# Optimization experiments

Hardware: AMD Instinct MI355X
Metric: run time of the kernel (lower is better)

## Reference

```python
import jax, jax.numpy as jnp
import numpy as np

SPH, SPW = 24, 24          # spatial tile size
NBLK = 2                   # channel blocks (in_channels // 512)
EPS = 1e-5


def _tiles(h, w):
    nh = int(np.ceil(h / SPH)); nw = int(np.ceil(w / SPW))
    sh = (h - SPH) // (nh - 1) if nh > 1 else 0
    sw = (w - SPW) // (nw - 1) if nw > 1 else 0
    offs = []
    for i in range(nh):
        for j in range(nw):
            offs.append((max(0, i * sh), max(0, j * sw)))
    return offs, nh, nw


def _mlp(x_v, w1, b1, w2, b2):
    # 1x1 conv1d pair over the spatial_area axis: x_v (B, S, C)
    h = jax.nn.relu(jnp.einsum('os,bsc->boc', w1, x_v) + b1[None, :, None])
    return jnp.einsum('so,boc->bsc', w2, h) + b2[None, :, None]


def _forward(x, w_in1, b_in1, w_in2, b_in2, w_out1, b_out1, w_out2, b_out2, bn_gamma, bn_beta):
    bt, c, h, w = x.shape
    offs, nh, nw = _tiles(h, w)
    # gather overlapping (here exactly tiling) spatial patches -> stacked chunk batch
    chunks = [x[:, :, ty:ty + SPH, tx:tx + SPW].reshape(bt, c, SPH * SPW) for ty, tx in offs]
    x_stacked = jnp.concatenate(chunks, 0)            # (nchunks*bt, c, S)
    x_v = jnp.transpose(x_stacked, (0, 2, 1))         # (B, S, c)
    x_v = _mlp(x_v, w_in1, b_in1, w_in2, b_in2)
    # negative squared-distance score over channel means (no detach in this branch)
    x_m = x_v.mean(axis=1)                            # (B, c)
    score = -(x_m[:, None, :] - x_m[:, :, None]) ** 2  # (B, c, c)
    blk = c // NBLK
    ids = jnp.arange(c) // blk
    mask = ids[:, None] == ids[None, :]               # block-diagonal channel mask
    score = jnp.where(mask[None], score, -jnp.inf)
    attn = jax.nn.softmax(score, axis=1)              # softmax over dim 1 (rows)
    out = jnp.einsum('bsc,bcd->bsd', x_v, attn)       # torch.bmm(x_v, attn)
    out = _mlp(out, w_out1, b_out1, w_out2, b_out2)
    # BatchNorm1d(spatial_area) in training mode: stats over (B, c) per S-channel
    mu = out.mean(axis=(0, 2), keepdims=True)
    var = out.var(axis=(0, 2), keepdims=True)
    out = (out - mu) * jax.lax.rsqrt(var + EPS) * bn_gamma[None, :, None] + bn_beta[None, :, None]
    out = jnp.transpose(out, (0, 2, 1))               # (B, c, S)
    # scatter_add chunks back (scaled by 1/spblock_h^2, as in the original)
    scale = 1.0 / (nh * nh)
    res = x
    for idx, (ty, tx) in enumerate(offs):
        chunk = out[idx * bt:(idx + 1) * bt].reshape(bt, c, SPH, SPW)
        res = res.at[:, :, ty:ty + SPH, tx:tx + SPW].add(chunk * scale)
    return jax.nn.relu(res)


def setup_inputs() -> dict:
    key = jax.random.key(0)
    ks = jax.random.split(key, 9)
    S = SPH * SPW          # 576
    H = S // 8             # 72 (reduction=8)
    s = 0.02
    return {
        'x': jax.random.normal(ks[0], (16, 1024, 48, 48), dtype=jnp.float32),
        'w_in1': jax.random.normal(ks[1], (H, S), dtype=jnp.float32) * s,
        'b_in1': jnp.zeros((H,), jnp.float32),
        'w_in2': jax.random.normal(ks[2], (S, H), dtype=jnp.float32) * s,
        'b_in2': jnp.zeros((S,), jnp.float32),
        'w_out1': jax.random.normal(ks[3], (H, S), dtype=jnp.float32) * s,
        'b_out1': jnp.zeros((H,), jnp.float32),
        'w_out2': jax.random.normal(ks[4], (S, H), dtype=jnp.float32) * s,
        'b_out2': jnp.zeros((S,), jnp.float32),
        'bn_gamma': jnp.ones((S,), jnp.float32),
        'bn_beta': jnp.zeros((S,), jnp.float32),
    }


def reference(x, w_in1, b_in1, w_in2, b_in2, w_out1, b_out1, w_out2, b_out2, bn_gamma, bn_beta):
    return _forward(x, w_in1, b_in1, w_in2, b_in2, w_out1, b_out1, w_out2, b_out2, bn_gamma, bn_beta)
```

## Files before the change

kernel.cpp:

```cpp
#include <hip/hip_runtime.h>
#include <hip/hip_bf16.h>


#define EPS 1e-5f

typedef __attribute__((ext_vector_type(8))) short short8;
typedef __attribute__((ext_vector_type(4))) short short4v;
typedef __attribute__((ext_vector_type(4))) float f32x4;
typedef __attribute__((ext_vector_type(4))) float float4v;

#define GLD_LDS(g, l) __builtin_amdgcn_global_load_lds( \
    (const __attribute__((address_space(1))) void*)(g), \
    (__attribute__((address_space(3))) void*)(l), 16, 0, 0)

static __device__ __forceinline__ unsigned short f2bu(float f) {
    union { __hip_bfloat16 h; unsigned short u; } cv;
    cv.h = __float2bfloat16(f);
    return cv.u;
}

__global__ void prep_k(const float* __restrict__ w_in1, const float* __restrict__ b_in1,
                       const float* __restrict__ w_in2,
                       const float* __restrict__ w_out1, const float* __restrict__ b_out1,
                       const float* __restrict__ w_out2,
                       __hip_bfloat16* __restrict__ w1p, __hip_bfloat16* __restrict__ w1op,
                       __hip_bfloat16* __restrict__ w2p, __hip_bfloat16* __restrict__ w2op,
                       float* __restrict__ b1p, float* __restrict__ b1op)
{
    int i = blockIdx.x * 256 + threadIdx.x;
    if (i < 128 * 576) {
        int r = i / 576, c = i - r * 576;
        w1p[i]  = __float2bfloat16(r < 72 ? w_in1[r * 576 + c] : 0.f);
        w1op[i] = __float2bfloat16(r < 72 ? w_out1[r * 576 + c] : 0.f);
    }
    if (i < 640 * 96) {
        int r = i / 96, c = i - r * 96;
        bool ok = (r < 576) && (c < 72);
        w2p[i]  = __float2bfloat16(ok ? w_in2[r * 72 + c] : 0.f);
        w2op[i] = __float2bfloat16(ok ? w_out2[r * 72 + c] : 0.f);
    }
    if (i < 128) {
        b1p[i]  = i < 72 ? b_in1[i] : 0.f;
        b1op[i] = i < 72 ? b_out1[i] : 0.f;
    }
}

__global__ void extract_k(const float4v* __restrict__ x4, __hip_bfloat16* __restrict__ xv)
{
    int i = blockIdx.x * 256 + threadIdx.x;
    int s4 = i % 144;
    int m = i / 144;
    int c = m & 1023;
    int b = m >> 10;
    int n = b & 15, ti = b >> 4;
    int ty = (ti >> 1) * 24, tx = (ti & 1) * 24;
    int s = s4 * 4;
    int sy = s / 24, sx = s - sy * 24;
    float4v v = x4[((((n << 10) + c) * 48 + ty + sy) * 48 + tx + sx) >> 2];
    short4v pk;
    pk.x = (short)f2bu(v.x); pk.y = (short)f2bu(v.y);
    pk.z = (short)f2bu(v.z); pk.w = (short)f2bu(v.w);
    *(short4v*)(xv + (long)i * 4) = pk;
}

template<int MODE>
__global__ __launch_bounds__(256) void fused_mlp(
    const unsigned short* __restrict__ A,
    const unsigned short* __restrict__ W1,
    const float* __restrict__ b1,
    const unsigned short* __restrict__ W2,
    const float* __restrict__ b2,
    __hip_bfloat16* __restrict__ xv1T,
    float* __restrict__ xm_raw,
    __hip_bfloat16* __restrict__ C,
    float* __restrict__ statsR)
{
    constexpr int SMEM_SH = (MODE == 0) ? 38016 : 21504;
    __shared__ __align__(16) unsigned short smem[SMEM_SH];
    unsigned short* As = smem;
    unsigned short* Bs = smem + 4096;
    unsigned short* Hs = smem + 8192;
    unsigned short* T  = smem + 21504;

    const int m0 = blockIdx.x * 128;
    const int t = threadIdx.x;
    const int lane = t & 63, wave = t >> 6;
    const int wr = wave >> 1, wc = wave & 1;
    const int lrow = lane & 15, kq = (lane >> 4) * 8;
    const int cr = (lane >> 4) * 4;
    const int r0 = t >> 2, c0 = (t & 3) * 8;

    f32x4 acc[4][4];
    #pragma unroll
    for (int i = 0; i < 4; ++i)
        #pragma unroll
        for (int j = 0; j < 4; ++j)
            acc[i][j] = (f32x4){0.f, 0.f, 0.f, 0.f};

    for (int k0 = 0; k0 < 576; k0 += 32) {
        GLD_LDS(A + (long)(m0 + r0) * 576 + k0 + c0,      &As[t * 8]);
        GLD_LDS(A + (long)(m0 + r0 + 64) * 576 + k0 + c0, &As[(t + 256) * 8]);
        GLD_LDS(W1 + (long)r0 * 576 + k0 + c0,            &Bs[t * 8]);
        GLD_LDS(W1 + (long)(r0 + 64) * 576 + k0 + c0,     &Bs[(t + 256) * 8]);
        __syncthreads();
        short8 af[4], bf[4];
        #pragma unroll
        for (int i = 0; i < 4; ++i)
            af[i] = *(const short8*)&As[(wr * 64 + i * 16 + lrow) * 32 + kq];
        #pragma unroll
        for (int j = 0; j < 4; ++j)
            bf[j] = *(const short8*)&Bs[(wc * 64 + j * 16 + lrow) * 32 + kq];
        #pragma unroll
        for (int i = 0; i < 4; ++i)
            #pragma unroll
            for (int j = 0; j < 4; ++j)
                acc[i][j] = __builtin_amdgcn_mfma_f32_16x16x32_bf16(af[i], bf[j], acc[i][j], 0, 0, 0);
        __syncthreads();
    }

    #pragma unroll
    for (int j = 0; j < 4; ++j) {
        int col = wc * 64 + j * 16 + lrow;
        if (col < 96) {
            float bv = b1[col];
            #pragma unroll
            for (int i = 0; i < 4; ++i) {
                int row = wr * 64 + i * 16 + cr;
                #pragma unroll
                for (int r = 0; r < 4; ++r)
                    Hs[(row + r) * 104 + col] = f2bu(fmaxf(acc[i][j][r] + bv, 0.f));
            }
        }
    }
    __syncthreads();

    float rsum[4][4];
    if (MODE == 0)
        #pragma unroll
        for (int i = 0; i < 4; ++i)
            #pragma unroll
            for (int r = 0; r < 4; ++r)
                rsum[i][r] = 0.f;

    const int z = m0 >> 9, m_local = m0 & 511;

    for (int n0 = 0; n0 < 640; n0 += 128) {
        f32x4 a2[4][4];
        #pragma unroll
        for (int i = 0; i < 4; ++i)
            #pragma unroll
            for (int j = 0; j < 4; ++j)
                a2[i][j] = (f32x4){0.f, 0.f, 0.f, 0.f};

        for (int k0 = 0; k0 < 96; k0 += 32) {
            GLD_LDS(W2 + (long)(n0 + r0) * 96 + k0 + c0,      &Bs[t * 8]);
            GLD_LDS(W2 + (long)(n0 + r0 + 64) * 96 + k0 + c0, &Bs[(t + 256) * 8]);
            __syncthreads();
            short8 af[4], bf[4];
            #pragma unroll
            for (int i = 0; i < 4; ++i)
                af[i] = *(const short8*)&Hs[(wr * 64 + i * 16 + lrow) * 104 + k0 + kq];
            #pragma unroll
            for (int j = 0; j < 4; ++j)
                bf[j] = *(const short8*)&Bs[(wc * 64 + j * 16 + lrow) * 32 + kq];
            #pragma unroll
            for (int i = 0; i < 4; ++i)
                #pragma unroll
                for (int j = 0; j < 4; ++j)
                    a2[i][j] = __builtin_amdgcn_mfma_f32_16x16x32_bf16(af[i], bf[j], a2[i][j], 0, 0, 0);
            __syncthreads();
        }

        if (MODE == 0) {
            #pragma unroll
            for (int i = 0; i < 4; ++i)
                #pragma unroll
                for (int r = 0; r < 4; ++r)
                    rsum[i][r] += a2[i][0][r] + a2[i][1][r] + a2[i][2][r] + a2[i][3][r];

            #pragma unroll
            for (int j = 0; j < 4; ++j) {
                int col = wc * 64 + j * 16 + lrow;
                float bv = (n0 + col < 576) ? b2[n0 + col] : 0.f;
                #pragma unroll
                for (int i = 0; i < 4; ++i) {
                    int row = wr * 64 + i * 16 + cr;
                    #pragma unroll
                    for (int r = 0; r < 4; ++r)
                        T[(row + r) * 129 + col] = f2bu(a2[i][j][r] + bv);
                }
            }
            __syncthreads();

            int s_r = t >> 1, chalf = (t & 1) * 64;
            if (n0 + s_r < 576) {
                __hip_bfloat16* dst = xv1T + ((long)z * 640 + n0 + s_r) * 512 + m_local + chalf;
                #pragma unroll
                for (int v8 = 0; v8 < 8; ++v8) {
                    short8 pk;
                    #pragma unroll
                    for (int e = 0; e < 8; ++e)
                        pk[e] = (short)T[(chalf + v8 * 8 + e) * 129 + s_r];
                    *(short8*)(dst + v8 * 8) = pk;
                }
            }
            __syncthreads();
        } else {
            float* st = statsR + (blockIdx.x & 7) * 1152;
            #pragma unroll
            for (int j = 0; j < 4; ++j) {
                int col = n0 + wc * 64 + j * 16 + lrow;
                bool live = col < 576;
                float bv = live ? b2[col] : 0.f;
                float s1 = 0.f, s2 = 0.f;
                #pragma unroll
                for (int i = 0; i < 4; ++i) {
                    long rowb = (long)(m0 + wr * 64 + i * 16 + cr) * 576;
                    #pragma unroll
                    for (int r = 0; r < 4; ++r) {
                        float v = a2[i][j][r] + bv;
                        s1 += v; s2 += v * v;
                        if (live) C[rowb + (long)r * 576 + col] = __float2bfloat16(v);
                    }
                }
                s1 += __shfl_xor(s1, 16, 64); s1 += __shfl_xor(s1, 32, 64);
                s2 += __shfl_xor(s2, 16, 64); s2 += __shfl_xor(s2, 32, 64);
                if ((lane >> 4) == 0 && live) {
                    atomicAdd(&st[col], s1);
                    atomicAdd(&st[576 + col], s2);
                }
            }
        }
    }

    if (MODE == 0) {
        #pragma unroll
        for (int i = 0; i < 4; ++i)
            #pragma unroll
            for (int r = 0; r < 4; ++r) {
                float v = rsum[i][r];
                v += __shfl_xor(v, 1, 64);
                v += __shfl_xor(v, 2, 64);
                v += __shfl_xor(v, 4, 64);
                v += __shfl_xor(v, 8, 64);
                if (lrow == 0)
                    atomicAdd(&xm_raw[m0 + wr * 64 + i * 16 + cr + r], v);
            }
    }
}

__global__ void denom_k(const float* __restrict__ xm_raw, const float* __restrict__ b_in2,
                        float* __restrict__ xmn, float* __restrict__ invd)
{
    __shared__ float sx[512];
    __shared__ float red[256];
    int z = blockIdx.x;
    int t = threadIdx.x;
    float p = 0.f;
    for (int i = t; i < 576; i += 256) p += b_in2[i];
    red[t] = p; __syncthreads();
    for (int o = 128; o; o >>= 1) { if (t < o) red[t] += red[t + o]; __syncthreads(); }
    float btot = red[0];
    for (int i = t; i < 512; i += 256) {
        float m = (xm_raw[(long)z * 512 + i] + btot) * (1.f / 576.f);
        sx[i] = m;
        xmn[(long)z * 512 + i] = m;
    }
    __syncthreads();
    #pragma unroll
    for (int dd = 0; dd < 2; ++dd) {
        int d = t + dd * 256;
        float xd = sx[d], s = 0.f;
        for (int c = 0; c < 512; ++c) { float df = sx[c] - xd; s += __expf(-df * df); }
        invd[(long)z * 512 + d] = 1.f / s;
    }
}

__global__ __launch_bounds__(256) void gemm_attn(
    const unsigned short* __restrict__ Bg,
    const float* __restrict__ xmn, const float* __restrict__ invd,
    __hip_bfloat16* __restrict__ C)
{
    __shared__ unsigned short As[128 * 32];
    __shared__ unsigned short Bs[128 * 32];
    __shared__ float sxm[512];
    __shared__ float sinv[128];
    int g = blockIdx.x;
    int xcd = g & 7, idx = g >> 3;
    int y = idx & 3;
    int combo = (idx >> 2) * 8 + xcd;
    int nx = combo % 5, z = combo / 5;
    const int m0 = y * 128, n0 = nx * 128;
    const int t = threadIdx.x;
    const int lane = t & 63, wave = t >> 6;
    const int wr = wave >> 1, wc = wave & 1;
    const int lrow = lane & 15, kq = (lane >> 4) * 8;
    const int r0 = t >> 2, c0 = (t & 3) * 8;
    const unsigned short* B = Bg + (long)z * 640 * 512;
    __hip_bfloat16* Cz = C + (long)z * 512 * 576;

    for (int i = t; i < 512; i += 256) sxm[i] = xmn[(long)z * 512 + i];
    if (t < 128) sinv[t] = invd[(long)z * 512 + m0 + t];
    __syncthreads();

    const int dA = t >> 1, cbA = (t & 1) * 16;
    const float xd = sxm[m0 + dA];
    const float ivd = sinv[dA];

    f32x4 acc[4][4];
    #pragma unroll
    for (int i = 0; i < 4; ++i)
        #pragma unroll
        for (int j = 0; j < 4; ++j)
            acc[i][j] = (f32x4){0.f, 0.f, 0.f, 0.f};

    for (int k0 = 0; k0 < 512; k0 += 32) {
        GLD_LDS(B + (long)(n0 + r0) * 512 + k0 + c0,      &Bs[t * 8]);
        GLD_LDS(B + (long)(n0 + r0 + 64) * 512 + k0 + c0, &Bs[(t + 256) * 8]);
        short8 pk0, pk1;
        #pragma unroll
        for (int e = 0; e < 8; ++e) {
            float d0 = sxm[k0 + cbA + e] - xd;
            pk0[e] = (short)f2bu(__expf(-d0 * d0) * ivd);
            float d1 = sxm[k0 + cbA + 8 + e] - xd;
            pk1[e] = (short)f2bu(__expf(-d1 * d1) * ivd);
        }
        *(short8*)&As[dA * 32 + cbA]     = pk0;
        *(short8*)&As[dA * 32 + cbA + 8] = pk1;
        __syncthreads();
        short8 af[4], bf[4];
        #pragma unroll
        for (int i = 0; i < 4; ++i)
            af[i] = *(const short8*)&As[(wr * 64 + i * 16 + lrow) * 32 + kq];
        #pragma unroll
        for (int j = 0; j < 4; ++j)
            bf[j] = *(const short8*)&Bs[(wc * 64 + j * 16 + lrow) * 32 + kq];
        #pragma unroll
        for (int i = 0; i < 4; ++i)
            #pragma unroll
            for (int j = 0; j < 4; ++j)
                acc[i][j] = __builtin_amdgcn_mfma_f32_16x16x32_bf16(af[i], bf[j], acc[i][j], 0, 0, 0);
        __syncthreads();
    }

    const int cr = (lane >> 4) * 4;
    #pragma unroll
    for (int j = 0; j < 4; ++j) {
        int col = n0 + wc * 64 + j * 16 + lrow;
        if (col >= 576) continue;
        #pragma unroll
        for (int i = 0; i < 4; ++i) {
            long rowb = (long)(m0 + wr * 64 + i * 16 + cr) * 576;
            #pragma unroll
            for (int r = 0; r < 4; ++r)
                Cz[rowb + (long)r * 576 + col] = __float2bfloat16(acc[i][j][r]);
        }
    }
}

__global__ void bnfin_k(const float* __restrict__ statsR,
                        const float* __restrict__ gamma, const float* __restrict__ beta,
                        float* __restrict__ ab)
{
    int s = threadIdx.x;
    float sum = 0.f, sq = 0.f;
    #pragma unroll
    for (int r = 0; r < 8; ++r) {
        sum += statsR[r * 1152 + s];
        sq  += statsR[r * 1152 + 576 + s];
    }
    float mu = sum * (1.f / 65536.f);
    float var = sq * (1.f / 65536.f) - mu * mu;
    float a = gamma[s] * rsqrtf(var + EPS);
    ab[s] = a;
    ab[576 + s] = beta[s] - mu * a;
}

__global__ void final_k(const float4v* __restrict__ x4, const __hip_bfloat16* __restrict__ out3,
                        const float* __restrict__ ab, float4v* __restrict__ out4)
{
    int i = blockIdx.x * 256 + threadIdx.x;
    int xx4 = i % 12; int t = i / 12;
    int y = t % 48; t /= 48;
    int c = t & 1023; int n = t >> 10;
    int xx = xx4 * 4;
    int ti = (y / 24) * 2 + (xx / 24);
    int b = ti * 16 + n;
    int s = (y % 24) * 24 + (xx % 24);
    const __hip_bfloat16* o3 = out3 + (((long)b << 10) + c) * 576 + s;
    float4v xv = x4[i];
    float4v o;
    #pragma unroll
    for (int e = 0; e < 4; ++e) {
        float v = __bfloat162float(o3[e]);
        float bn = v * ab[s + e] + ab[576 + s + e];
        float r = (e == 0 ? xv.x : e == 1 ? xv.y : e == 2 ? xv.z : xv.w) + 0.25f * bn;
        if (e == 0) o.x = fmaxf(r, 0.f);
        else if (e == 1) o.y = fmaxf(r, 0.f);
        else if (e == 2) o.z = fmaxf(r, 0.f);
        else o.w = fmaxf(r, 0.f);
    }
    out4[i] = o;
}

extern "C" void kernel_launch(void* const* d_in, const int* in_sizes, int n_in,
                              void* d_out, int out_size, void* d_ws, size_t ws_size,
                              hipStream_t stream)
{
    const float* x      = (const float*)d_in[0];
    const float* w_in1  = (const float*)d_in[1];
    const float* b_in1  = (const float*)d_in[2];
    const float* w_in2  = (const float*)d_in[3];
    const float* b_in2  = (const float*)d_in[4];
    const float* w_out1 = (const float*)d_in[5];
    const float* b_out1 = (const float*)d_in[6];
    const float* w_out2 = (const float*)d_in[7];
    const float* b_out2 = (const float*)d_in[8];
    const float* gamma  = (const float*)d_in[9];
    const float* beta   = (const float*)d_in[10];

    char* ws = (char*)d_ws;
    __hip_bfloat16* xv0    = (__hip_bfloat16*)(ws);
    __hip_bfloat16* out3   = (__hip_bfloat16*)(ws + 88080384L);
    __hip_bfloat16* xv1T   = (__hip_bfloat16*)(ws + 163577856L);
    float*          xmn    = (float*)(ws + 247463936L);
    float*          xm_raw = (float*)(ws + 247726080L);
    float*          invd   = (float*)(ws + 247988224L);
    float*          statsR = (float*)(ws + 248250368L);
    float*          ab     = (float*)(ws + 248287232L);
    __hip_bfloat16* w1p    = (__hip_bfloat16*)(ws + 248291840L);
    __hip_bfloat16* w1op   = (__hip_bfloat16*)(ws + 248439296L);
    __hip_bfloat16* w2p    = (__hip_bfloat16*)(ws + 248586752L);
    __hip_bfloat16* w2op   = (__hip_bfloat16*)(ws + 248709632L);
    float*          b1p    = (float*)(ws + 248832512L);
    float*          b1op   = (float*)(ws + 248833024L);
    __hip_bfloat16* out2   = xv0;

    hipMemsetAsync(xm_raw, 0, 262144, stream);
    hipMemsetAsync(statsR, 0, 36864, stream);

    prep_k<<<288, 256, 0, stream>>>(w_in1, b_in1, w_in2, w_out1, b_out1, w_out2,
                                    w1p, w1op, w2p, w2op, b1p, b1op);

    extract_k<<<36864, 256, 0, stream>>>((const float4v*)x, xv0);

    fused_mlp<0><<<512, 256, 0, stream>>>(
        (const unsigned short*)xv0, (const unsigned short*)w1p, b1p,
        (const unsigned short*)w2p, b_in2,
        xv1T, xm_raw, nullptr, nullptr);

    denom_k<<<128, 256, 0, stream>>>(xm_raw, b_in2, xmn, invd);

    gemm_attn<<<2560, 256, 0, stream>>>(
        (const unsigned short*)xv1T, xmn, invd, out2);

    fused_mlp<1><<<512, 256, 0, stream>>>(
        (const unsigned short*)out2, (const unsigned short*)w1op, b1op,
        (const unsigned short*)w2op, b_out2,
        nullptr, nullptr, out3, statsR);

    bnfin_k<<<1, 576, 0, stream>>>(statsR, gamma, beta, ab);

    final_k<<<36864, 256, 0, stream>>>((const float4v*)x, out3, ab, (float4v*)d_out);
}
```

Baseline: 562.9 us.

## Reassociate attention with output MLP first layer to shrink intermediate GEMM

The attention bmm is reassociated so that the first output-MLP weight (72x576) is applied to x_v before attention, producing a small 128x512 G matrix per chunk. The full 576x512 transposed x_v intermediate is no longer materialised, and the attention GEMM inner dimension drops from 576 to 128 rows. The attention GEMM is also fused with the second output-MLP layer and the BN statistics, which removes one kernel and one large bf16 round trip. The cost is an extra GEMM inside the first MLP kernel and more LDS per block, which may reduce occupancy.

```diff
diff --git a/kernel.cpp b/kernel.cpp
--- a/kernel.cpp
+++ b/kernel.cpp
@@ -23,21 +23,24 @@
                        const float* __restrict__ w_in2,
                        const float* __restrict__ w_out1, const float* __restrict__ b_out1,
                        const float* __restrict__ w_out2,
-                       __hip_bfloat16* __restrict__ w1p, __hip_bfloat16* __restrict__ w1op,
-                       __hip_bfloat16* __restrict__ w2p, __hip_bfloat16* __restrict__ w2op,
+                       __hip_bfloat16* __restrict__ w1p, __hip_bfloat16* __restrict__ w2p,
+                       __hip_bfloat16* __restrict__ w2op, __hip_bfloat16* __restrict__ w1oq,
                        float* __restrict__ b1p, float* __restrict__ b1op)
 {
     int i = blockIdx.x * 256 + threadIdx.x;
     if (i < 128 * 576) {
         int r = i / 576, c = i - r * 576;
-        w1p[i]  = __float2bfloat16(r < 72 ? w_in1[r * 576 + c] : 0.f);
-        w1op[i] = __float2bfloat16(r < 72 ? w_out1[r * 576 + c] : 0.f);
+        w1p[i] = __float2bfloat16(r < 72 ? w_in1[r * 576 + c] : 0.f);
     }
     if (i < 640 * 96) {
         int r = i / 96, c = i - r * 96;
         bool ok = (r < 576) && (c < 72);
         w2p[i]  = __float2bfloat16(ok ? w_in2[r * 72 + c] : 0.f);
         w2op[i] = __float2bfloat16(ok ? w_out2[r * 72 + c] : 0.f);
+    }
+    if (i < 128 * 640) {
+        int r = i / 640, c = i - r * 640;
+        w1oq[i] = __float2bfloat16((r < 72 && c < 576) ? w_out1[r * 576 + c] : 0.f);
     }
     if (i < 128) {
         b1p[i]  = i < 72 ? b_in1[i] : 0.f;
@@ -63,20 +66,17 @@
     *(short4v*)(xv + (long)i * 4) = pk;
 }
 
-template<int MODE>
-__global__ __launch_bounds__(256) void fused_mlp(
+__global__ __launch_bounds__(256) void fused_mlp1G(
     const unsigned short* __restrict__ A,
     const unsigned short* __restrict__ W1,
     const float* __restrict__ b1,
     const unsigned short* __restrict__ W2,
     const float* __restrict__ b2,
-    __hip_bfloat16* __restrict__ xv1T,
-    float* __restrict__ xm_raw,
-    __hip_bfloat16* __restrict__ C,
-    float* __restrict__ statsR)
-{
-    constexpr int SMEM_SH = (MODE == 0) ? 38016 : 21504;
-    __shared__ __align__(16) unsigned short smem[SMEM_SH];
+    const unsigned short* __restrict__ W1O,
+    unsigned short* __restrict__ G,
+    float* __restrict__ xm_raw)
+{
+    __shared__ __align__(16) unsigned short smem[4096 + 4096 + 13312 + 17408];
     unsigned short* As = smem;
     unsigned short* Bs = smem + 4096;
     unsigned short* Hs = smem + 8192;
@@ -135,12 +135,18 @@
     __syncthreads();
 
     float rsum[4][4];
-    if (MODE == 0)
-        #pragma unroll
-        for (int i = 0; i < 4; ++i)
-            #pragma unroll
-            for (int r = 0; r < 4; ++r)
-                rsum[i][r] = 0.f;
+    #pragma unroll
+    for (int i = 0; i < 4; ++i)
+        #pragma unroll
+        for (int r = 0; r < 4; ++r)
+            rsum[i][r] = 0.f;
+
+    f32x4 gacc[4][4];
+    #pragma unroll
+    for (int i = 0; i < 4; ++i)
+        #pragma unroll
+        for (int j = 0; j < 4; ++j)
+            gacc[i][j] = (f32x4){0.f, 0.f, 0.f, 0.f};
 
     const int z = m0 >> 9, m_local = m0 & 511;
 
@@ -171,81 +177,70 @@
             __syncthreads();
         }
 
-        if (MODE == 0) {
+        #pragma unroll
+        for (int i = 0; i < 4; ++i)
+            #pragma unroll
+            for (int r = 0; r < 4; ++r)
+                rsum[i][r] += a2[i][0][r] + a2[i][1][r] + a2[i][2][r] + a2[i][3][r];
+
+        #pragma unroll
+        for (int j = 0; j < 4; ++j) {
+            int col = wc * 64 + j * 16 + lrow;
+            float bv = (n0 + col < 576) ? b2[n0 + col] : 0.f;
+            #pragma unroll
+            for (int i = 0; i < 4; ++i) {
+                int row = wr * 64 + i * 16 + cr;
+                #pragma unroll
+                for (int r = 0; r < 4; ++r)
+                    T[(row + r) * 136 + col] = f2bu(a2[i][j][r] + bv);
+            }
+        }
+        __syncthreads();
+
+        for (int kk = 0; kk < 128; kk += 32) {
+            GLD_LDS(W1O + (long)r0 * 640 + n0 + kk + c0,        &As[t * 8]);
+            GLD_LDS(W1O + (long)(r0 + 64) * 640 + n0 + kk + c0, &As[(t + 256) * 8]);
+            __syncthreads();
+            short8 af[4], bf[4];
             #pragma unroll
             for (int i = 0; i < 4; ++i)
-                #pragma unroll
-                for (int r = 0; r < 4; ++r)
-                    rsum[i][r] += a2[i][0][r] + a2[i][1][r] + a2[i][2][r] + a2[i][3][r];
-
-            #pragma unroll
-            for (int j = 0; j < 4; ++j) {
-                int col = wc * 64 + j * 16 + lrow;
-                float bv = (n0 + col < 576) ? b2[n0 + col] : 0.f;
-                #pragma unroll
-                for (int i = 0; i < 4; ++i) {
-                    int row = wr * 64 + i * 16 + cr;
-                    #pragma unroll
-                    for (int r = 0; r < 4; ++r)
-                        T[(row + r) * 129 + col] = f2bu(a2[i][j][r] + bv);
-                }
-            }
+                af[i] = *(const short8*)&As[(wr * 64 + i * 16 + lrow) * 32 + kq];
+            #pragma unroll
+            for (int j = 0; j < 4; ++j)
+                bf[j] = *(const short8*)&T[(wc * 64 + j * 16 + lrow) * 136 + kk + kq];
+            #pragma unroll
+            for (int i = 0; i < 4; ++i)
+                #pragma unroll
+                for (int j = 0; j < 4; ++j)
+                    gacc[i][j] = __builtin_amdgcn_mfma_f32_16x16x32_bf16(af[i], bf[j], gacc[i][j], 0, 0, 0);
             __syncthreads();
-
-            int s_r = t >> 1, chalf = (t & 1) * 64;
-            if (n0 + s_r < 576) {
-                __hip_bfloat16* dst = xv1T + ((long)z * 640 + n0 + s_r) * 512 + m_local + chalf;
-                #pragma unroll
-                for (int v8 = 0; v8 < 8; ++v8) {
-                    short8 pk;
-                    #pragma unroll
-                    for (int e = 0; e < 8; ++e)
-                        pk[e] = (short)T[(chalf + v8 * 8 + e) * 129 + s_r];
-                    *(short8*)(dst + v8 * 8) = pk;
-                }
-            }
-            __syncthreads();
-        } else {
-            float* st = statsR + (blockIdx.x & 7) * 1152;
-            #pragma unroll
-            for (int j = 0; j < 4; ++j) {
-                int col = n0 + wc * 64 + j * 16 + lrow;
-                bool live = col < 576;
-                float bv = live ? b2[col] : 0.f;
-                float s1 = 0.f, s2 = 0.f;
-                #pragma unroll
-                for (int i = 0; i < 4; ++i) {
-                    long rowb = (long)(m0 + wr * 64 + i * 16 + cr) * 576;
-                    #pragma unroll
-                    for (int r = 0; r < 4; ++r) {
-                        float v = a2[i][j][r] + bv;
-                        s1 += v; s2 += v * v;
-                        if (live) C[rowb + (long)r * 576 + col] = __float2bfloat16(v);
-                    }
-                }
-                s1 += __shfl_xor(s1, 16, 64); s1 += __shfl_xor(s1, 32, 64);
-                s2 += __shfl_xor(s2, 16, 64); s2 += __shfl_xor(s2, 32, 64);
-                if ((lane >> 4) == 0 && live) {
-                    atomicAdd(&st[col], s1);
-                    atomicAdd(&st[576 + col], s2);
-                }
-            }
-        }
-    }
-
-    if (MODE == 0) {
-        #pragma unroll
-        for (int i = 0; i < 4; ++i)
-            #pragma unroll
-            for (int r = 0; r < 4; ++r) {
-                float v = rsum[i][r];
-                v += __shfl_xor(v, 1, 64);
-                v += __shfl_xor(v, 2, 64);
-                v += __shfl_xor(v, 4, 64);
-                v += __shfl_xor(v, 8, 64);
-                if (lrow == 0)
-                    atomicAdd(&xm_raw[m0 + wr * 64 + i * 16 + cr + r], v);
-            }
+        }
+    }
+
+    #pragma unroll
+    for (int i = 0; i < 4; ++i)
+        #pragma unroll
+        for (int r = 0; r < 4; ++r) {
+            float v = rsum[i][r];
+            v += __shfl_xor(v, 1, 64);
+            v += __shfl_xor(v, 2, 64);
+            v += __shfl_xor(v, 4, 64);
+            v += __shfl_xor(v, 8, 64);
+            if (lrow == 0)
+                atomicAdd(&xm_raw[m0 + wr * 64 + i * 16 + cr + r], v);
+        }
+
+    unsigned short* Gz = G + (long)z * 128 * 512;
+    #pragma unroll
+    for (int j = 0; j < 4; ++j) {
+        int cn = wc * 64 + j * 16 + lrow;
+        #pragma unroll
+        for (int i = 0; i < 4; ++i) {
+            int h = wr * 64 + i * 16 + cr;
+            #pragma unroll
+            for (int r = 0; r < 4; ++r)
+                Gz[(long)(h + r) * 512 + m_local + cn] = f2bu(gacc[i][j][r]);
+        }
     }
 }
 
@@ -276,28 +271,33 @@
     }
 }
 
-__global__ __launch_bounds__(256) void gemm_attn(
-    const unsigned short* __restrict__ Bg,
+__global__ __launch_bounds__(256) void fused_attn_mlp2(
+    const unsigned short* __restrict__ G,
     const float* __restrict__ xmn, const float* __restrict__ invd,
-    __hip_bfloat16* __restrict__ C)
-{
-    __shared__ unsigned short As[128 * 32];
-    __shared__ unsigned short Bs[128 * 32];
+    const float* __restrict__ b1,
+    const unsigned short* __restrict__ W2,
+    const float* __restrict__ b2,
+    __hip_bfloat16* __restrict__ C,
+    float* __restrict__ statsR)
+{
+    __shared__ __align__(16) unsigned short smem[4096 + 4096 + 13312];
+    unsigned short* As = smem;
+    unsigned short* Bs = smem + 4096;
+    unsigned short* Hs = smem + 8192;
     __shared__ float sxm[512];
     __shared__ float sinv[128];
-    int g = blockIdx.x;
-    int xcd = g & 7, idx = g >> 3;
-    int y = idx & 3;
-    int combo = (idx >> 2) * 8 + xcd;
-    int nx = combo % 5, z = combo / 5;
-    const int m0 = y * 128, n0 = nx * 128;
+
+    int bid = blockIdx.x;
+    int lb = (bid & 7) * 64 + (bid >> 3);
+    int z = lb >> 2;
+    const int m0 = (lb & 3) * 128;
     const int t = threadIdx.x;
     const int lane = t & 63, wave = t >> 6;
     const int wr = wave >> 1, wc = wave & 1;
     const int lrow = lane & 15, kq = (lane >> 4) * 8;
+    const int cr = (lane >> 4) * 4;
     const int r0 = t >> 2, c0 = (t & 3) * 8;
-    const unsigned short* B = Bg + (long)z * 640 * 512;
-    __hip_bfloat16* Cz = C + (long)z * 512 * 576;
+    const unsigned short* Gz = G + (long)z * 128 * 512;
 
     for (int i = t; i < 512; i += 256) sxm[i] = xmn[(long)z * 512 + i];
     if (t < 128) sinv[t] = invd[(long)z * 512 + m0 + t];
@@ -315,8 +315,8 @@
             acc[i][j] = (f32x4){0.f, 0.f, 0.f, 0.f};
 
     for (int k0 = 0; k0 < 512; k0 += 32) {
-        GLD_LDS(B + (long)(n0 + r0) * 512 + k0 + c0,      &Bs[t * 8]);
-        GLD_LDS(B + (long)(n0 + r0 + 64) * 512 + k0 + c0, &Bs[(t + 256) * 8]);
+        GLD_LDS(Gz + (long)r0 * 512 + k0 + c0,        &Bs[t * 8]);
+        GLD_LDS(Gz + (long)(r0 + 64) * 512 + k0 + c0, &Bs[(t + 256) * 8]);
         short8 pk0, pk1;
         #pragma unroll
         for (int e = 0; e < 8; ++e) {
@@ -343,17 +343,73 @@
         __syncthreads();
     }
 
-    const int cr = (lane >> 4) * 4;
     #pragma unroll
     for (int j = 0; j < 4; ++j) {
-        int col = n0 + wc * 64 + j * 16 + lrow;
-        if (col >= 576) continue;
-        #pragma unroll
-        for (int i = 0; i < 4; ++i) {
-            long rowb = (long)(m0 + wr * 64 + i * 16 + cr) * 576;
-            #pragma unroll
-            for (int r = 0; r < 4; ++r)
-                Cz[rowb + (long)r * 576 + col] = __float2bfloat16(acc[i][j][r]);
+        int col = wc * 64 + j * 16 + lrow;
+        if (col < 96) {
+            float bv = b1[col];
+            #pragma unroll
+            for (int i = 0; i < 4; ++i) {
+                int row = wr * 64 + i * 16 + cr;
+                #pragma unroll
+                for (int r = 0; r < 4; ++r)
+                    Hs[(row + r) * 104 + col] = f2bu(fmaxf(acc[i][j][r] + bv, 0.f));
+            }
+        }
+    }
+    __syncthreads();
+
+    const long mg = (long)z * 512 + m0;
+    float* st = statsR + (bid & 7) * 1152;
+    for (int n0 = 0; n0 < 640; n0 += 128) {
+        f32x4 a2[4][4];
+        #pragma unroll
+        for (int i = 0; i < 4; ++i)
+            #pragma unroll
+            for (int j = 0; j < 4; ++j)
+                a2[i][j] = (f32x4){0.f, 0.f, 0.f, 0.f};
+
+        for (int k0 = 0; k0 < 96; k0 += 32) {
+            GLD_LDS(W2 + (long)(n0 + r0) * 96 + k0 + c0,      &Bs[t * 8]);
+            GLD_LDS(W2 + (long)(n0 + r0 + 64) * 96 + k0 + c0, &Bs[(t + 256) * 8]);
+            __syncthreads();
+            short8 af[4], bf[4];
+            #pragma unroll
+            for (int i = 0; i < 4; ++i)
+                af[i] = *(const short8*)&Hs[(wr * 64 + i * 16 + lrow) * 104 + k0 + kq];
+            #pragma unroll
+            for (int j = 0; j < 4; ++j)
+                bf[j] = *(const short8*)&Bs[(wc * 64 + j * 16 + lrow) * 32 + kq];
+            #pragma unroll
+            for (int i = 0; i < 4; ++i)
+                #pragma unroll
+                for (int j = 0; j < 4; ++j)
+                    a2[i][j] = __builtin_amdgcn_mfma_f32_16x16x32_bf16(af[i], bf[j], a2[i][j], 0, 0, 0);
+            __syncthreads();
+        }
+
+        #pragma unroll
+        for (int j = 0; j < 4; ++j) {
+            int col = n0 + wc * 64 + j * 16 + lrow;
+            bool live = col < 576;
+            float bv = live ? b2[col] : 0.f;
+            float s1 = 0.f, s2 = 0.f;
+            #pragma unroll
+            for (int i = 0; i < 4; ++i) {
+                long rowb = (mg + wr * 64 + i * 16 + cr) * 576;
+                #pragma unroll
+                for (int r = 0; r < 4; ++r) {
+                    float v = a2[i][j][r] + bv;
+                    s1 += v; s2 += v * v;
+                    if (live) C[rowb + (long)r * 576 + col] = __float2bfloat16(v);
+                }
+            }
+            s1 += __shfl_xor(s1, 16, 64); s1 += __shfl_xor(s1, 32, 64);
+            s2 += __shfl_xor(s2, 16, 64); s2 += __shfl_xor(s2, 32, 64);
+            if ((lane >> 4) == 0 && live) {
+                atomicAdd(&st[col], s1);
+                atomicAdd(&st[576 + col], s2);
+            }
         }
     }
 }
@@ -421,43 +477,38 @@
 
     char* ws = (char*)d_ws;
     __hip_bfloat16* xv0    = (__hip_bfloat16*)(ws);
-    __hip_bfloat16* out3   = (__hip_bfloat16*)(ws + 88080384L);
-    __hip_bfloat16* xv1T   = (__hip_bfloat16*)(ws + 163577856L);
-    float*          xmn    = (float*)(ws + 247463936L);
-    float*          xm_raw = (float*)(ws + 247726080L);
-    float*          invd   = (float*)(ws + 247988224L);
-    float*          statsR = (float*)(ws + 248250368L);
-    float*          ab     = (float*)(ws + 248287232L);
-    __hip_bfloat16* w1p    = (__hip_bfloat16*)(ws + 248291840L);
-    __hip_bfloat16* w1op   = (__hip_bfloat16*)(ws + 248439296L);
-    __hip_bfloat16* w2p    = (__hip_bfloat16*)(ws + 248586752L);
-    __hip_bfloat16* w2op   = (__hip_bfloat16*)(ws + 248709632L);
-    float*          b1p    = (float*)(ws + 248832512L);
-    float*          b1op   = (float*)(ws + 248833024L);
-    __hip_bfloat16* out2   = xv0;
+    __hip_bfloat16* out3   = (__hip_bfloat16*)(ws + 75497472L);
+    unsigned short* G      = (unsigned short*)(ws + 150994944L);
+    float*          xmn    = (float*)(ws + 167772160L);
+    float*          xm_raw = (float*)(ws + 168034304L);
+    float*          invd   = (float*)(ws + 168296448L);
+    float*          statsR = (float*)(ws + 168558592L);
+    float*          ab     = (float*)(ws + 168595456L);
+    __hip_bfloat16* w1p    = (__hip_bfloat16*)(ws + 168600064L);
+    __hip_bfloat16* w2p    = (__hip_bfloat16*)(ws + 168747520L);
+    __hip_bfloat16* w2op   = (__hip_bfloat16*)(ws + 168870400L);
+    __hip_bfloat16* w1oq   = (__hip_bfloat16*)(ws + 168993280L);
+    float*          b1p    = (float*)(ws + 169157120L);
+    float*          b1op   = (float*)(ws + 169157632L);
 
     hipMemsetAsync(xm_raw, 0, 262144, stream);
     hipMemsetAsync(statsR, 0, 36864, stream);
 
-    prep_k<<<288, 256, 0, stream>>>(w_in1, b_in1, w_in2, w_out1, b_out1, w_out2,
-                                    w1p, w1op, w2p, w2op, b1p, b1op);
+    prep_k<<<320, 256, 0, stream>>>(w_in1, b_in1, w_in2, w_out1, b_out1, w_out2,
+                                    w1p, w2p, w2op, w1oq, b1p, b1op);
 
     extract_k<<<36864, 256, 0, stream>>>((const float4v*)x, xv0);
 
-    fused_mlp<0><<<512, 256, 0, stream>>>(
+    fused_mlp1G<<<512, 256, 0, stream>>>(
         (const unsigned short*)xv0, (const unsigned short*)w1p, b1p,
-        (const unsigned short*)w2p, b_in2,
-        xv1T, xm_raw, nullptr, nullptr);
+        (const unsigned short*)w2p, b_in2, (const unsigned short*)w1oq,
+        G, xm_raw);
 
     denom_k<<<128, 256, 0, stream>>>(xm_raw, b_in2, xmn, invd);
 
-    gemm_attn<<<2560, 256, 0, stream>>>(
-        (const unsigned short*)xv1T, xmn, invd, out2);
-
-    fused_mlp<1><<<512, 256, 0, stream>>>(
-        (const unsigned short*)out2, (const unsigned short*)w1op, b1op,
-        (const unsigned short*)w2op, b_out2,
-        nullptr, nullptr, out3, statsR);
+    fused_attn_mlp2<<<512, 256, 0, stream>>>(
+        G, xmn, invd, b1op, (const unsigned short*)w2op, b_out2,
+        out3, statsR);
 
     bnfin_k<<<1, 576, 0, stream>>>(statsR, gamma, beta, ab);
 
```

After: 517.2 us. 8.1% less time.
